# Kernel optimization log

Hardware: AMD Instinct MI355X
Metric: run time of the kernel (lower is better)

The kernel has to match this reference:

```python
import jax, jax.numpy as jnp
import numpy as np

B, N, E, ENT, D, H, L = 64, 2048, 32768, 100000, 256, 256, 512


def setup_inputs() -> dict:
    key = jax.random.key(0)
    ks = jax.random.split(key, 12)
    return {
        "neighbors": jax.random.randint(ks[0], (B, N), 0, ENT),
        "adj_row": jax.random.randint(ks[1], (B, E), 0, N),
        "adj_col": jax.random.randint(ks[2], (B, E), 0, N),
        "adj_val": jax.random.uniform(ks[3], (B, E), dtype=jnp.float32),
        "emb_table": jax.random.normal(ks[4], (ENT, D), dtype=jnp.float32),
        "W1": jax.random.normal(ks[5], (D, H), dtype=jnp.float32) * (1.0 / np.sqrt(H)),
        "b1": jax.random.normal(ks[6], (H,), dtype=jnp.float32) * 0.01,
        "W2": jax.random.normal(ks[7], (H, H), dtype=jnp.float32) * (1.0 / np.sqrt(H)),
        "b2": jax.random.normal(ks[8], (H,), dtype=jnp.float32) * 0.01,
        "fc1_w": jax.random.normal(ks[9], (H, H), dtype=jnp.float32) * (1.0 / np.sqrt(H)),
        "fc1_b": jax.random.normal(ks[10], (H,), dtype=jnp.float32) * 0.01,
        "cur_len": L,
    }


def _gcn_layer(x, W, b, adj_row, adj_col, adj_val):
    # x: [B,N,din] -> support: [B,N,dout]
    support = jnp.einsum("bnd,dh->bnh", x, W)
    # sparse adj @ support: gather columns, scale by edge value, scatter-add to rows
    gathered = jnp.take_along_axis(support, adj_col[:, :, None], axis=1)  # [B,E,h]
    weighted = gathered * adj_val[:, :, None]
    agg = jax.vmap(lambda r, g: jax.ops.segment_sum(g, r, num_segments=N))(adj_row, weighted)
    return agg + b


def reference(neighbors, adj_row, adj_col, adj_val, emb_table, W1, b1, W2, b2, fc1_w, fc1_b, cur_len):
    x = emb_table[neighbors]                                   # [B,N,D] embedding gather
    x = _gcn_layer(x, W1, b1, adj_row, adj_col, adj_val)       # GCN layer 1
    x = _gcn_layer(x, W2, b2, adj_row, adj_col, adj_val)       # GCN layer 2
    seq = x[:, :cur_len, :]                                    # keep cur_node prefix, padded to common L
    pooled = jnp.mean(seq, axis=1, keepdims=True)              # self.seq == 'mean'
    return jax.nn.relu(jnp.einsum("blh,ho->blo", pooled, fc1_w) + fc1_b)  # [B,1,H]
```

## Files before the change

kernel.cpp:

```cpp
#include <hip/hip_runtime.h>

#define B 64
#define N 2048
#define E 32768
#define D 256
#define H 256
#define GCH 32
#define SEG 8
#define EPB (E / SEG)

__global__ __launch_bounds__(512) void edge_w_kernel(
    const int* __restrict__ adj_row, const int* __restrict__ adj_col,
    const float* __restrict__ adj_val, const int* __restrict__ cur_len,
    float* __restrict__ w_part, float* __restrict__ sw_part)
{
    __shared__ float wloc[N];
    __shared__ float sred[8];
    const int b = blockIdx.x, seg = blockIdx.y, tid = threadIdx.x;
    const int L = *cur_len;

    ((float4*)wloc)[tid] = make_float4(0.f, 0.f, 0.f, 0.f);
    __syncthreads();

    const int base = b * E + seg * EPB;
    const int4*   row4 = (const int4*)  (adj_row + base);
    const int4*   col4 = (const int4*)  (adj_col + base);
    const float4* val4 = (const float4*)(adj_val + base);

    float svp = 0.f;
    #pragma unroll
    for (int k = 0; k < EPB / (512 * 4); ++k) {
        const int    i = tid + k * 512;
        const int4   r = row4[i];
        const int4   c = col4[i];
        const float4 v = val4[i];
        if (r.x < L) { atomicAdd(&wloc[c.x], v.x); svp += v.x; }
        if (r.y < L) { atomicAdd(&wloc[c.y], v.y); svp += v.y; }
        if (r.z < L) { atomicAdd(&wloc[c.z], v.z); svp += v.z; }
        if (r.w < L) { atomicAdd(&wloc[c.w], v.w); svp += v.w; }
    }
    __syncthreads();

    float4* dst = (float4*)(w_part + ((size_t)b * SEG + seg) * N);
    dst[tid] = ((const float4*)wloc)[tid];

    for (int off = 32; off; off >>= 1) svp += __shfl_down(svp, off, 64);
    if ((tid & 63) == 0) sred[tid >> 6] = svp;
    __syncthreads();
    if (tid == 0) {
        float s = 0.f;
        #pragma unroll
        for (int i = 0; i < 8; ++i) s += sred[i];
        sw_part[b * SEG + seg] = s;
    }
}

__global__ __launch_bounds__(512) void edge_z_kernel(
    const int* __restrict__ adj_row, const int* __restrict__ adj_col,
    const float* __restrict__ adj_val, const float* __restrict__ w_part,
    float* __restrict__ z_part)
{
    __shared__ float wfull[N];
    __shared__ float zloc[N];
    const int b = blockIdx.x, seg = blockIdx.y, tid = threadIdx.x;

    const float4* wp4 = (const float4*)(w_part + (size_t)b * SEG * N);
    float4 s = make_float4(0.f, 0.f, 0.f, 0.f);
    #pragma unroll
    for (int sg = 0; sg < SEG; ++sg) {
        const float4 v = wp4[sg * (N / 4) + tid];
        s.x += v.x; s.y += v.y; s.z += v.z; s.w += v.w;
    }
    ((float4*)wfull)[tid] = s;
    ((float4*)zloc)[tid]  = make_float4(0.f, 0.f, 0.f, 0.f);
    __syncthreads();

    const int base = b * E + seg * EPB;
    const int4*   row4 = (const int4*)  (adj_row + base);
    const int4*   col4 = (const int4*)  (adj_col + base);
    const float4* val4 = (const float4*)(adj_val + base);

    #pragma unroll
    for (int k = 0; k < EPB / (512 * 4); ++k) {
        const int    i = tid + k * 512;
        const int4   r = row4[i];
        const int4   c = col4[i];
        const float4 v = val4[i];
        float wv;
        wv = wfull[r.x]; if (wv != 0.f) atomicAdd(&zloc[c.x], wv * v.x);
        wv = wfull[r.y]; if (wv != 0.f) atomicAdd(&zloc[c.y], wv * v.y);
        wv = wfull[r.z]; if (wv != 0.f) atomicAdd(&zloc[c.z], wv * v.z);
        wv = wfull[r.w]; if (wv != 0.f) atomicAdd(&zloc[c.w], wv * v.w);
    }
    __syncthreads();

    float4* dst = (float4*)(z_part + ((size_t)b * SEG + seg) * N);
    dst[tid] = ((const float4*)zloc)[tid];
}

__global__ __launch_bounds__(256) void gather_kernel(
    const int* __restrict__ neighbors, const float* __restrict__ emb,
    const float* __restrict__ z_part, float* __restrict__ u_part)
{
    const int b = blockIdx.x, grp = blockIdx.y, tid = threadIdx.x;
    const int lane = tid & 63, rg = tid >> 6;
    const int n0 = grp * 64;

    __shared__ float zh[2][64];
    __shared__ int   ns[64];
    if (tid < 128) {
        const int j = tid & 63, half = tid >> 6;
        float s = 0.f;
        #pragma unroll
        for (int sg = 0; sg < SEG / 2; ++sg)
            s += z_part[((size_t)b * SEG + half * (SEG / 2) + sg) * N + n0 + j];
        zh[half][j] = s;
        if (half == 0) ns[j] = neighbors[(size_t)b * N + n0 + j];
    }
    __syncthreads();

    const float4* __restrict__ emb4 = (const float4*)emb;

    float4 v[16];
    #pragma unroll
    for (int i = 0; i < 16; ++i) {
        const int j = i * 4 + rg;
        v[i] = emb4[(size_t)ns[j] * (D / 4) + lane];
    }

    float4 acc = make_float4(0.f, 0.f, 0.f, 0.f);
    #pragma unroll
    for (int i = 0; i < 16; ++i) {
        const int j = i * 4 + rg;
        const float zv = zh[0][j] + zh[1][j];
        acc.x += zv * v[i].x; acc.y += zv * v[i].y;
        acc.z += zv * v[i].z; acc.w += zv * v[i].w;
    }

    __shared__ float4 red[256];
    red[tid] = acc;
    __syncthreads();
    if (tid < 64) {
        float4 a = red[tid], bb = red[tid + 64], c = red[tid + 128], d = red[tid + 192];
        float4 s = make_float4(a.x + bb.x + c.x + d.x, a.y + bb.y + c.y + d.y,
                               a.z + bb.z + c.z + d.z, a.w + bb.w + c.w + d.w);
        ((float4*)u_part)[((size_t)b * GCH + grp) * (D / 4) + tid] = s;
    }
}

__global__ __launch_bounds__(1024) void head_kernel(
    const float* __restrict__ u_part, const float* __restrict__ sw_part,
    const float* __restrict__ W1, const float* __restrict__ b1,
    const float* __restrict__ W2, const float* __restrict__ b2,
    const float* __restrict__ fc1_w, const float* __restrict__ fc1_b,
    const int* __restrict__ cur_len, float* __restrict__ out)
{
    const int b = blockIdx.x;
    const int t = threadIdx.x & 255;
    const int s = threadIdx.x >> 8;
    __shared__ float red[4][256];
    __shared__ float su[D];
    __shared__ float sy[H];
    __shared__ float sp[H];

    float part = 0.f;
    #pragma unroll
    for (int c = 0; c < GCH / 4; ++c)
        part += u_part[((size_t)b * GCH + s * (GCH / 4) + c) * D + t];
    red[s][t] = part;
    __syncthreads();
    if (s == 0) su[t] = red[0][t] + red[1][t] + red[2][t] + red[3][t];
    __syncthreads();

    part = 0.f;
    #pragma unroll 8
    for (int k = 0; k < 64; ++k) {
        const int d = s * 64 + k;
        part += su[d] * W1[d * H + t];
    }
    red[s][t] = part;
    __syncthreads();
    if (s == 0) {
        float sw = 0.f;
        #pragma unroll
        for (int i = 0; i < SEG; ++i) sw += sw_part[b * SEG + i];
        sy[t] = red[0][t] + red[1][t] + red[2][t] + red[3][t] + sw * b1[t];
    }
    __syncthreads();

    const float invL = 1.f / (float)(*cur_len);
    part = 0.f;
    #pragma unroll 8
    for (int k = 0; k < 64; ++k) {
        const int d = s * 64 + k;
        part += sy[d] * W2[d * H + t];
    }
    red[s][t] = part;
    __syncthreads();
    if (s == 0)
        sp[t] = (red[0][t] + red[1][t] + red[2][t] + red[3][t]) * invL + b2[t];
    __syncthreads();

    part = 0.f;
    #pragma unroll 8
    for (int k = 0; k < 64; ++k) {
        const int d = s * 64 + k;
        part += sp[d] * fc1_w[d * H + t];
    }
    red[s][t] = part;
    __syncthreads();
    if (s == 0) {
        const float v = red[0][t] + red[1][t] + red[2][t] + red[3][t] + fc1_b[t];
        out[(size_t)b * H + t] = fmaxf(v, 0.f);
    }
}

extern "C" void kernel_launch(void* const* d_in, const int* in_sizes, int n_in,
                              void* d_out, int out_size, void* d_ws, size_t ws_size,
                              hipStream_t stream) {
    const int*   neighbors = (const int*)  d_in[0];
    const int*   adj_row   = (const int*)  d_in[1];
    const int*   adj_col   = (const int*)  d_in[2];
    const float* adj_val   = (const float*)d_in[3];
    const float* emb_table = (const float*)d_in[4];
    const float* W1        = (const float*)d_in[5];
    const float* b1        = (const float*)d_in[6];
    const float* W2        = (const float*)d_in[7];
    const float* b2        = (const float*)d_in[8];
    const float* fc1_w     = (const float*)d_in[9];
    const float* fc1_b     = (const float*)d_in[10];
    const int*   cur_len   = (const int*)  d_in[11];
    float*       out       = (float*)d_out;

    float* wp_ws = (float*)d_ws;
    float* zp_ws = wp_ws + (size_t)B * SEG * N;
    float* sw_ws = zp_ws + (size_t)B * SEG * N;
    float* u_ws  = sw_ws + (size_t)B * SEG;

    edge_w_kernel<<<dim3(B, SEG), 512, 0, stream>>>(adj_row, adj_col, adj_val,
                                                    cur_len, wp_ws, sw_ws);
    edge_z_kernel<<<dim3(B, SEG), 512, 0, stream>>>(adj_row, adj_col, adj_val,
                                                    wp_ws, zp_ws);
    gather_kernel<<<dim3(B, GCH), 256, 0, stream>>>(neighbors, emb_table, zp_ws, u_ws);
    head_kernel<<<B, 1024, 0, stream>>>(u_ws, sw_ws, W1, b1, W2, b2,
                                        fc1_w, fc1_b, cur_len, out);
}
```

Baseline: 222.7 us.

## Prefetch embedding table into cache using extra blocks in edge kernels

Doubles the grid of both edge kernels, and the extra blocks stream the whole 100000x256 float embedding table, half in each kernel, writing only a checksum to a sink buffer. The aim is to bring the table into the last-level cache while the atomic-bound edge passes run, so the random-row gather kernel later hits cache instead of HBM. The cost is reading about 100MB of extra memory traffic, which competes with the edge kernels for bandwidth and may not fit in cache at all.

```diff
diff --git a/kernel.cpp b/kernel.cpp
--- a/kernel.cpp
+++ b/kernel.cpp
@@ -5,18 +5,37 @@
 #define E 32768
 #define D 256
 #define H 256
+#define ENT 100000
 #define GCH 32
 #define SEG 8
 #define EPB (E / SEG)
 
+#define EMB4      (ENT * (D / 4))
+#define EMB4_HALF (EMB4 / 2)
+
 __global__ __launch_bounds__(512) void edge_w_kernel(
     const int* __restrict__ adj_row, const int* __restrict__ adj_col,
     const float* __restrict__ adj_val, const int* __restrict__ cur_len,
+    const float* __restrict__ emb, float* __restrict__ warm_sink,
     float* __restrict__ w_part, float* __restrict__ sw_part)
 {
     __shared__ float wloc[N];
     __shared__ float sred[8];
     const int b = blockIdx.x, seg = blockIdx.y, tid = threadIdx.x;
+
+    if (seg >= SEG) {
+        const float4* __restrict__ e4 = (const float4*)emb;
+        const int wb = b * SEG + (seg - SEG);
+        float s = 0.f;
+        for (size_t i = (size_t)wb * 512 + tid; i < (size_t)EMB4_HALF;
+             i += (size_t)512 * 512) {
+            const float4 v = e4[i];
+            s += v.x + v.y + v.z + v.w;
+        }
+        warm_sink[wb] = s;
+        return;
+    }
+
     const int L = *cur_len;
 
     ((float4*)wloc)[tid] = make_float4(0.f, 0.f, 0.f, 0.f);
@@ -58,11 +77,25 @@
 __global__ __launch_bounds__(512) void edge_z_kernel(
     const int* __restrict__ adj_row, const int* __restrict__ adj_col,
     const float* __restrict__ adj_val, const float* __restrict__ w_part,
+    const float* __restrict__ emb, float* __restrict__ warm_sink,
     float* __restrict__ z_part)
 {
     __shared__ float wfull[N];
     __shared__ float zloc[N];
     const int b = blockIdx.x, seg = blockIdx.y, tid = threadIdx.x;
+
+    if (seg >= SEG) {
+        const float4* __restrict__ e4 = (const float4*)emb;
+        const int wb = b * SEG + (seg - SEG);
+        float s = 0.f;
+        for (size_t i = (size_t)EMB4_HALF + (size_t)wb * 512 + tid;
+             i < (size_t)EMB4; i += (size_t)512 * 512) {
+            const float4 v = e4[i];
+            s += v.x + v.y + v.z + v.w;
+        }
+        warm_sink[512 + wb] = s;
+        return;
+    }
 
     const float4* wp4 = (const float4*)(w_part + (size_t)b * SEG * N);
     float4 s = make_float4(0.f, 0.f, 0.f, 0.f);
@@ -236,11 +269,14 @@
     float* zp_ws = wp_ws + (size_t)B * SEG * N;
     float* sw_ws = zp_ws + (size_t)B * SEG * N;
     float* u_ws  = sw_ws + (size_t)B * SEG;
-
-    edge_w_kernel<<<dim3(B, SEG), 512, 0, stream>>>(adj_row, adj_col, adj_val,
-                                                    cur_len, wp_ws, sw_ws);
-    edge_z_kernel<<<dim3(B, SEG), 512, 0, stream>>>(adj_row, adj_col, adj_val,
-                                                    wp_ws, zp_ws);
+    float* sink  = u_ws  + (size_t)B * GCH * D;
+
+    edge_w_kernel<<<dim3(B, 2 * SEG), 512, 0, stream>>>(adj_row, adj_col, adj_val,
+                                                        cur_len, emb_table, sink,
+                                                        wp_ws, sw_ws);
+    edge_z_kernel<<<dim3(B, 2 * SEG), 512, 0, stream>>>(adj_row, adj_col, adj_val,
+                                                        wp_ws, emb_table, sink,
+                                                        zp_ws);
     gather_kernel<<<dim3(B, GCH), 256, 0, stream>>>(neighbors, emb_table, zp_ws, u_ws);
     head_kernel<<<B, 1024, 0, stream>>>(u_ws, sw_ws, W1, b1, W2, b2,
                                         fc1_w, fc1_b, cur_len, out);
```

Measured after the change: 230.7 us. 3.6% more time.

## Invert embedding gather into per-entity scan with slot index

Applied to the files above, without the earlier changes.

Adds kernels that zero a per-entity count array and scatter each (batch, node) position into up to 16 slots per entity id. The embedding contraction then walks entity ranges, so each used table row is read once and contiguously, and its z-weighted contribution is accumulated per batch with shared-memory atomics. Per-block partials are reduced in the head kernel. This trades the random 1KB row gathers (one per position, duplicates included) for extra launches, global and LDS atomics, scattered z_part reads, and a larger partial-sum buffer. Correctness silently depends on no entity appearing more than 16 times across the batch.

```diff
diff --git a/kernel.cpp b/kernel.cpp
--- a/kernel.cpp
+++ b/kernel.cpp
@@ -5,9 +5,29 @@
 #define E 32768
 #define D 256
 #define H 256
-#define GCH 32
+#define ENT 100000
 #define SEG 8
 #define EPB (E / SEG)
+#define GCH 32
+#define SLOTS 16
+#define GSB 256
+#define ENT_PB ((ENT + GSB - 1) / GSB)
+
+__global__ __launch_bounds__(512) void zero_cnt_kernel(int* __restrict__ cnt)
+{
+    const int i = blockIdx.x * 512 + threadIdx.x;
+    if (i < ENT / 4) ((int4*)cnt)[i] = make_int4(0, 0, 0, 0);
+}
+
+__global__ __launch_bounds__(512) void scatter_kernel(
+    const int* __restrict__ neighbors, int* __restrict__ cnt,
+    unsigned int* __restrict__ slot)
+{
+    const int i = blockIdx.x * 512 + threadIdx.x;
+    const int e = neighbors[i];
+    const int p = atomicAdd(&cnt[e], 1);
+    if (p < SLOTS) slot[(size_t)e * SLOTS + p] = (unsigned int)i;
+}
 
 __global__ __launch_bounds__(512) void edge_w_kernel(
     const int* __restrict__ adj_row, const int* __restrict__ adj_col,
@@ -98,58 +118,65 @@
     dst[tid] = ((const float4*)zloc)[tid];
 }
 
-__global__ __launch_bounds__(256) void gather_kernel(
-    const int* __restrict__ neighbors, const float* __restrict__ emb,
-    const float* __restrict__ z_part, float* __restrict__ u_part)
-{
-    const int b = blockIdx.x, grp = blockIdx.y, tid = threadIdx.x;
-    const int lane = tid & 63, rg = tid >> 6;
-    const int n0 = grp * 64;
-
-    __shared__ float zh[2][64];
-    __shared__ int   ns[64];
-    if (tid < 128) {
-        const int j = tid & 63, half = tid >> 6;
-        float s = 0.f;
-        #pragma unroll
-        for (int sg = 0; sg < SEG / 2; ++sg)
-            s += z_part[((size_t)b * SEG + half * (SEG / 2) + sg) * N + n0 + j];
-        zh[half][j] = s;
-        if (half == 0) ns[j] = neighbors[(size_t)b * N + n0 + j];
-    }
+__global__ __launch_bounds__(512) void gather_scan_kernel(
+    const int* __restrict__ cnt, const unsigned int* __restrict__ slot,
+    const float* __restrict__ z_part, const float* __restrict__ emb,
+    float* __restrict__ u_pp)
+{
+    __shared__ float uacc[4][B][64];
+    const int k = blockIdx.x, tid = threadIdx.x;
+    const int wv = tid >> 6, lane = tid & 63;
+
+    for (int x = tid; x < 4 * B * 64; x += 512) ((float*)uacc)[x] = 0.f;
     __syncthreads();
 
     const float4* __restrict__ emb4 = (const float4*)emb;
-
-    float4 v[16];
-    #pragma unroll
-    for (int i = 0; i < 16; ++i) {
-        const int j = i * 4 + rg;
-        v[i] = emb4[(size_t)ns[j] * (D / 4) + lane];
-    }
-
-    float4 acc = make_float4(0.f, 0.f, 0.f, 0.f);
-    #pragma unroll
-    for (int i = 0; i < 16; ++i) {
-        const int j = i * 4 + rg;
-        const float zv = zh[0][j] + zh[1][j];
-        acc.x += zv * v[i].x; acc.y += zv * v[i].y;
-        acc.z += zv * v[i].z; acc.w += zv * v[i].w;
-    }
-
-    __shared__ float4 red[256];
-    red[tid] = acc;
-    __syncthreads();
-    if (tid < 64) {
-        float4 a = red[tid], bb = red[tid + 64], c = red[tid + 128], d = red[tid + 192];
-        float4 s = make_float4(a.x + bb.x + c.x + d.x, a.y + bb.y + c.y + d.y,
-                               a.z + bb.z + c.z + d.z, a.w + bb.w + c.w + d.w);
-        ((float4*)u_part)[((size_t)b * GCH + grp) * (D / 4) + tid] = s;
+    const int e0 = k * ENT_PB;
+    const int e1 = min(e0 + ENT_PB, ENT);
+
+    for (int e = e0 + wv; e < e1; e += 16) {
+        const int eB = e + 8;
+        const int cA = min(cnt[e], SLOTS);
+        const int cB = (eB < e1) ? min(cnt[eB], SLOTS) : 0;
+        float4 rA = make_float4(0.f, 0.f, 0.f, 0.f), rB = rA;
+        if (cA) rA = emb4[(size_t)e  * (D / 4) + lane];
+        if (cB) rB = emb4[(size_t)eB * (D / 4) + lane];
+
+        for (int r = 0; r < cA; ++r) {
+            const unsigned int pl = slot[(size_t)e * SLOTS + r];
+            const int pb = pl >> 11, pn = pl & 2047;
+            const float* zp = z_part + (size_t)pb * (SEG * N) + pn;
+            float zv = 0.f;
+            #pragma unroll
+            for (int sg = 0; sg < SEG; ++sg) zv += zp[sg * N];
+            atomicAdd(&uacc[0][pb][lane], zv * rA.x);
+            atomicAdd(&uacc[1][pb][lane], zv * rA.y);
+            atomicAdd(&uacc[2][pb][lane], zv * rA.z);
+            atomicAdd(&uacc[3][pb][lane], zv * rA.w);
+        }
+        for (int r = 0; r < cB; ++r) {
+            const unsigned int pl = slot[(size_t)eB * SLOTS + r];
+            const int pb = pl >> 11, pn = pl & 2047;
+            const float* zp = z_part + (size_t)pb * (SEG * N) + pn;
+            float zv = 0.f;
+            #pragma unroll
+            for (int sg = 0; sg < SEG; ++sg) zv += zp[sg * N];
+            atomicAdd(&uacc[0][pb][lane], zv * rB.x);
+            atomicAdd(&uacc[1][pb][lane], zv * rB.y);
+            atomicAdd(&uacc[2][pb][lane], zv * rB.z);
+            atomicAdd(&uacc[3][pb][lane], zv * rB.w);
+        }
+    }
+    __syncthreads();
+
+    for (int x = tid; x < B * D; x += 512) {
+        const int bb = x >> 8, d = x & 255;
+        u_pp[((size_t)k * B + bb) * D + d] = uacc[d & 3][bb][d >> 2];
     }
 }
 
 __global__ __launch_bounds__(1024) void head_kernel(
-    const float* __restrict__ u_part, const float* __restrict__ sw_part,
+    const float* __restrict__ u_pp, const float* __restrict__ sw_part,
     const float* __restrict__ W1, const float* __restrict__ b1,
     const float* __restrict__ W2, const float* __restrict__ b2,
     const float* __restrict__ fc1_w, const float* __restrict__ fc1_b,
@@ -164,9 +191,9 @@
     __shared__ float sp[H];
 
     float part = 0.f;
-    #pragma unroll
-    for (int c = 0; c < GCH / 4; ++c)
-        part += u_part[((size_t)b * GCH + s * (GCH / 4) + c) * D + t];
+    #pragma unroll 8
+    for (int kk = s * (GSB / 4); kk < (s + 1) * (GSB / 4); ++kk)
+        part += u_pp[((size_t)kk * B + b) * D + t];
     red[s][t] = part;
     __syncthreads();
     if (s == 0) su[t] = red[0][t] + red[1][t] + red[2][t] + red[3][t];
@@ -235,13 +262,18 @@
     float* wp_ws = (float*)d_ws;
     float* zp_ws = wp_ws + (size_t)B * SEG * N;
     float* sw_ws = zp_ws + (size_t)B * SEG * N;
-    float* u_ws  = sw_ws + (size_t)B * SEG;
-
+    float* up_ws = sw_ws + (size_t)B * SEG;
+    int*   cnt_ws  = (int*)(up_ws + (size_t)GSB * B * D);
+    unsigned int* slot_ws = (unsigned int*)(cnt_ws + ENT);
+
+    zero_cnt_kernel<<<(ENT / 4 + 511) / 512, 512, 0, stream>>>(cnt_ws);
+    scatter_kernel<<<(B * N) / 512, 512, 0, stream>>>(neighbors, cnt_ws, slot_ws);
     edge_w_kernel<<<dim3(B, SEG), 512, 0, stream>>>(adj_row, adj_col, adj_val,
                                                     cur_len, wp_ws, sw_ws);
     edge_z_kernel<<<dim3(B, SEG), 512, 0, stream>>>(adj_row, adj_col, adj_val,
                                                     wp_ws, zp_ws);
-    gather_kernel<<<dim3(B, GCH), 256, 0, stream>>>(neighbors, emb_table, zp_ws, u_ws);
-    head_kernel<<<B, 1024, 0, stream>>>(u_ws, sw_ws, W1, b1, W2, b2,
+    gather_scan_kernel<<<GSB, 512, 0, stream>>>(cnt_ws, slot_ws, zp_ws,
+                                                emb_table, up_ws);
+    head_kernel<<<B, 1024, 0, stream>>>(up_ws, sw_ws, W1, b1, W2, b2,
                                         fc1_w, fc1_b, cur_len, out);
 }
```

Result: slower. 398.9 us (+79.1%).

## Replace per-batch embedding gather with scatter to dense Z and dense GEMM over table

Applied to the files above, without the earlier changes.

Instead of gathering 2048 embedding rows per batch and weighting them, node weights are scattered into a dense [B, ENT] coefficient matrix Z, and a streaming GEMM Z @ emb_table reads the whole table once across all batches. The aim is to turn 131k random row gathers into one sequential pass over the 100MB table. In exchange it adds zeroing of a 25MB Z buffer, atomic scatters, and a dense GEMM of about 13 GFLOP in FP32 on CUDA cores, along with partial-sum reduction over 256 blocks in the head.

```diff
diff --git a/kernel.cpp b/kernel.cpp
--- a/kernel.cpp
+++ b/kernel.cpp
@@ -5,19 +5,33 @@
 #define E 32768
 #define D 256
 #define H 256
-#define GCH 32
+#define ENT 100000
 #define SEG 8
 #define EPB (E / SEG)
+#define KPAD 100352
+#define KCH 392
+#define GB 256
+#define Z4PB 3136
 
 __global__ __launch_bounds__(512) void edge_w_kernel(
     const int* __restrict__ adj_row, const int* __restrict__ adj_col,
     const float* __restrict__ adj_val, const int* __restrict__ cur_len,
-    float* __restrict__ w_part, float* __restrict__ sw_part)
+    float* __restrict__ Z, float* __restrict__ w_part,
+    float* __restrict__ sw_part)
 {
     __shared__ float wloc[N];
     __shared__ float sred[8];
     const int b = blockIdx.x, seg = blockIdx.y, tid = threadIdx.x;
     const int L = *cur_len;
+
+    {
+        float4* z4 = (float4*)Z + (size_t)(b * SEG + seg) * Z4PB;
+        #pragma unroll
+        for (int k = 0; k < 7; ++k) {
+            const int x = tid + k * 512;
+            if (x < Z4PB) z4[x] = make_float4(0.f, 0.f, 0.f, 0.f);
+        }
+    }
 
     ((float4*)wloc)[tid] = make_float4(0.f, 0.f, 0.f, 0.f);
     __syncthreads();
@@ -98,58 +112,63 @@
     dst[tid] = ((const float4*)zloc)[tid];
 }
 
-__global__ __launch_bounds__(256) void gather_kernel(
-    const int* __restrict__ neighbors, const float* __restrict__ emb,
-    const float* __restrict__ z_part, float* __restrict__ u_part)
-{
-    const int b = blockIdx.x, grp = blockIdx.y, tid = threadIdx.x;
-    const int lane = tid & 63, rg = tid >> 6;
-    const int n0 = grp * 64;
-
-    __shared__ float zh[2][64];
-    __shared__ int   ns[64];
-    if (tid < 128) {
-        const int j = tid & 63, half = tid >> 6;
-        float s = 0.f;
-        #pragma unroll
-        for (int sg = 0; sg < SEG / 2; ++sg)
-            s += z_part[((size_t)b * SEG + half * (SEG / 2) + sg) * N + n0 + j];
-        zh[half][j] = s;
-        if (half == 0) ns[j] = neighbors[(size_t)b * N + n0 + j];
-    }
-    __syncthreads();
-
-    const float4* __restrict__ emb4 = (const float4*)emb;
-
-    float4 v[16];
-    #pragma unroll
-    for (int i = 0; i < 16; ++i) {
-        const int j = i * 4 + rg;
-        v[i] = emb4[(size_t)ns[j] * (D / 4) + lane];
-    }
-
-    float4 acc = make_float4(0.f, 0.f, 0.f, 0.f);
-    #pragma unroll
-    for (int i = 0; i < 16; ++i) {
-        const int j = i * 4 + rg;
-        const float zv = zh[0][j] + zh[1][j];
-        acc.x += zv * v[i].x; acc.y += zv * v[i].y;
-        acc.z += zv * v[i].z; acc.w += zv * v[i].w;
-    }
-
-    __shared__ float4 red[256];
-    red[tid] = acc;
-    __syncthreads();
-    if (tid < 64) {
-        float4 a = red[tid], bb = red[tid + 64], c = red[tid + 128], d = red[tid + 192];
-        float4 s = make_float4(a.x + bb.x + c.x + d.x, a.y + bb.y + c.y + d.y,
-                               a.z + bb.z + c.z + d.z, a.w + bb.w + c.w + d.w);
-        ((float4*)u_part)[((size_t)b * GCH + grp) * (D / 4) + tid] = s;
-    }
+__global__ __launch_bounds__(512) void scatter_kernel(
+    const int* __restrict__ neighbors, const float* __restrict__ z_part,
+    float* __restrict__ Z)
+{
+    const int i = blockIdx.x * 512 + threadIdx.x;
+    const int b = i >> 11, n = i & 2047;
+    const float* zp = z_part + (size_t)b * (SEG * N) + n;
+    float zv = 0.f;
+    #pragma unroll
+    for (int sg = 0; sg < SEG; ++sg) zv += zp[sg * N];
+    atomicAdd(&Z[(size_t)b * KPAD + neighbors[i]], zv);
+}
+
+__global__ __launch_bounds__(256) void gemm_kernel(
+    const float* __restrict__ Z, const float* __restrict__ emb,
+    float* __restrict__ u_pp)
+{
+    const int blk = blockIdx.x;
+    const int g   = threadIdx.x >> 6;
+    const int q   = threadIdx.x & 63;
+    const int k0  = blk * KCH;
+    const float4* __restrict__ e4 = (const float4*)emb;
+
+    float4 acc[16];
+    #pragma unroll
+    for (int i = 0; i < 16; ++i) acc[i] = make_float4(0.f, 0.f, 0.f, 0.f);
+
+    const float* __restrict__ zb = Z + (size_t)(g * 16) * KPAD + k0;
+
+    for (int k = 0; k < KCH; k += 4) {
+        const int kk = k0 + k;
+        float4 a[16];
+        #pragma unroll
+        for (int i = 0; i < 16; ++i)
+            a[i] = *(const float4*)(zb + (size_t)i * KPAD + k);
+        float4 e0_ = make_float4(0.f,0.f,0.f,0.f), e1_ = e0_, e2_ = e0_, e3_ = e0_;
+        if (kk + 0 < ENT) e0_ = e4[(size_t)(kk + 0) * (D / 4) + q];
+        if (kk + 1 < ENT) e1_ = e4[(size_t)(kk + 1) * (D / 4) + q];
+        if (kk + 2 < ENT) e2_ = e4[(size_t)(kk + 2) * (D / 4) + q];
+        if (kk + 3 < ENT) e3_ = e4[(size_t)(kk + 3) * (D / 4) + q];
+        #pragma unroll
+        for (int i = 0; i < 16; ++i) {
+            acc[i].x += a[i].x*e0_.x + a[i].y*e1_.x + a[i].z*e2_.x + a[i].w*e3_.x;
+            acc[i].y += a[i].x*e0_.y + a[i].y*e1_.y + a[i].z*e2_.y + a[i].w*e3_.y;
+            acc[i].z += a[i].x*e0_.z + a[i].y*e1_.z + a[i].z*e2_.z + a[i].w*e3_.z;
+            acc[i].w += a[i].x*e0_.w + a[i].y*e1_.w + a[i].z*e2_.w + a[i].w*e3_.w;
+        }
+    }
+
+    float4* dst = (float4*)u_pp + (size_t)blk * (B * D / 4);
+    #pragma unroll
+    for (int i = 0; i < 16; ++i)
+        dst[(g * 16 + i) * (D / 4) + q] = acc[i];
 }
 
 __global__ __launch_bounds__(1024) void head_kernel(
-    const float* __restrict__ u_part, const float* __restrict__ sw_part,
+    const float* __restrict__ u_pp, const float* __restrict__ sw_part,
     const float* __restrict__ W1, const float* __restrict__ b1,
     const float* __restrict__ W2, const float* __restrict__ b2,
     const float* __restrict__ fc1_w, const float* __restrict__ fc1_b,
@@ -164,9 +183,9 @@
     __shared__ float sp[H];
 
     float part = 0.f;
-    #pragma unroll
-    for (int c = 0; c < GCH / 4; ++c)
-        part += u_part[((size_t)b * GCH + s * (GCH / 4) + c) * D + t];
+    #pragma unroll 8
+    for (int c = s * (GB / 4); c < (s + 1) * (GB / 4); ++c)
+        part += u_pp[(size_t)c * (B * D) + b * D + t];
     red[s][t] = part;
     __syncthreads();
     if (s == 0) su[t] = red[0][t] + red[1][t] + red[2][t] + red[3][t];
@@ -235,13 +254,15 @@
     float* wp_ws = (float*)d_ws;
     float* zp_ws = wp_ws + (size_t)B * SEG * N;
     float* sw_ws = zp_ws + (size_t)B * SEG * N;
-    float* u_ws  = sw_ws + (size_t)B * SEG;
+    float* Z_ws  = sw_ws + (size_t)B * SEG;
+    float* up_ws = Z_ws  + (size_t)B * KPAD;
 
     edge_w_kernel<<<dim3(B, SEG), 512, 0, stream>>>(adj_row, adj_col, adj_val,
-                                                    cur_len, wp_ws, sw_ws);
+                                                    cur_len, Z_ws, wp_ws, sw_ws);
     edge_z_kernel<<<dim3(B, SEG), 512, 0, stream>>>(adj_row, adj_col, adj_val,
                                                     wp_ws, zp_ws);
-    gather_kernel<<<dim3(B, GCH), 256, 0, stream>>>(neighbors, emb_table, zp_ws, u_ws);
-    head_kernel<<<B, 1024, 0, stream>>>(u_ws, sw_ws, W1, b1, W2, b2,
+    scatter_kernel<<<(B * N) / 512, 512, 0, stream>>>(neighbors, zp_ws, Z_ws);
+    gemm_kernel<<<GB, 256, 0, stream>>>(Z_ws, emb_table, up_ws);
+    head_kernel<<<B, 1024, 0, stream>>>(up_ws, sw_ws, W1, b1, W2, b2,
                                         fc1_w, fc1_b, cur_len, out);
 }
```

New measurement: 331.0 us. 48.6% more time.
